# Performance work log

Hardware: AMD Instinct MI355X
Metric: run time of the kernel (lower is better)

Reference implementation:

```python
import jax, jax.numpy as jnp
import numpy as np

N_EMB = 512
EMB_DIM = 64
DECAY = 0.99
EPS = 1e-5


def setup_inputs() -> dict:
    key = jax.random.key(0)
    k1, k2 = jax.random.split(key)
    x = jax.random.normal(k1, (32, EMB_DIM, 64, 64), dtype=jnp.float32)
    weight = jax.random.uniform(k2, (EMB_DIM, N_EMB), dtype=jnp.float32)  # rd_init=True: torch.rand(emb_dim, n_emb)
    cluster_size = jnp.zeros((N_EMB,), dtype=jnp.float32)
    embed_avg = weight  # buffer initialized as embed.clone()
    return {"x": x, "weight": weight, "cluster_size": cluster_size, "embed_avg": embed_avg}


def reference(x, weight, cluster_size, embed_avg):
    B, D, H, W = x.shape
    n_emb = weight.shape[1]
    # (B, D, H, W) -> (N, D) tokens
    flat = jnp.transpose(x, (0, 2, 3, 1)).reshape(-1, D)
    dist = (jnp.sum(flat * flat, axis=1, keepdims=True)
            - 2.0 * (flat @ weight)
            + jnp.sum(weight * weight, axis=0)[None, :])
    argmin = jnp.argmin(dist, axis=1)                      # (N,)
    quant = jnp.take(weight.T, argmin, axis=0)             # gather -> (N, D)
    result = jnp.transpose(quant.reshape(B, H, W, D), (0, 3, 1, 2))  # (B, D, H, W)

    # --- EMA codebook update (training branch) ---
    ones = jnp.ones(argmin.shape, dtype=x.dtype)
    n_idx = jax.ops.segment_sum(ones, argmin, num_segments=n_emb)    # onehot.sum(0)
    n_idx = jnp.where(n_idx == 0, jnp.ones_like(n_idx), n_idx)       # clamp empty clusters to 1
    new_cluster_size = DECAY * cluster_size + (1.0 - DECAY) * n_idx
    embed_sum = jax.ops.segment_sum(flat, argmin, num_segments=n_emb).T  # flatten.T @ onehot -> (D, n_emb)
    new_embed_avg = DECAY * embed_avg + (1.0 - DECAY) * embed_sum
    n = jnp.sum(new_cluster_size)
    cs = (new_cluster_size + EPS) / (n + n_emb * EPS) * n
    new_weight = new_embed_avg / cs[None, :]

    return result, argmin.reshape(B, H, W), new_weight, new_cluster_size, new_embed_avg
```

## Files before the change

kernel.cpp:

```cpp
#include <hip/hip_runtime.h>

#define NEMB 512
#define EMB 64
#define BSTR 262144
#define DECAYF 0.99f
#define OMDF 0.01f
#define EPSF 1e-5f
#define GAP_T 0.012f

typedef __attribute__((ext_vector_type(8))) short bf16x8;
typedef __attribute__((ext_vector_type(4))) float f32x4;

__device__ __forceinline__ unsigned short f2bf(float f) {
    unsigned u = __float_as_uint(f);
    return (unsigned short)((u + 0x7FFFu + ((u >> 16) & 1u)) >> 16);
}
__device__ __forceinline__ float bf2f(unsigned short h) {
    return __uint_as_float(((unsigned)h) << 16);
}

__global__ void prep_kernel(const float* __restrict__ w,
                            unsigned short* __restrict__ wh, unsigned short* __restrict__ wl,
                            float* __restrict__ wsq,
                            float* __restrict__ cnt_ws, float* __restrict__ es_region) {
    int j = threadIdx.x;
    if (blockIdx.x < 8) {
        int d0 = blockIdx.x << 3;
        bf16x8 hb, lb;
#pragma unroll
        for (int i = 0; i < 8; ++i) {
            float v = w[(d0 + i) * NEMB + j];
            unsigned short h = f2bf(v);
            hb[i] = (short)h;
            lb[i] = (short)f2bf(v - bf2f(h));
        }
        *(bf16x8*)(wh + j * EMB + d0) = hb;
        *(bf16x8*)(wl + j * EMB + d0) = lb;
    } else {
        float s = 0.f;
#pragma unroll
        for (int d = 0; d < EMB; ++d) { float v = w[d * NEMB + j]; s = fmaf(v, v, s); }
        wsq[j] = s;
        cnt_ws[j] = 0.f;
#pragma unroll
        for (int k = j; k < 32768; k += 512) es_region[k] = 0.f;
    }
}

#define UPD(S1, J1, S2, J2, s_, j_) do { \
    if (s_ < S1 || (s_ == S1 && j_ < J1)) { S2 = S1; J2 = J1; S1 = s_; J1 = j_; } \
    else if (s_ < S2 || (s_ == S2 && j_ < J2)) { S2 = s_; J2 = j_; } } while (0)

__global__ __launch_bounds__(256, 4) void vq_main(
    const float* __restrict__ x, const float* __restrict__ w,
    const unsigned short* __restrict__ wh, const unsigned short* __restrict__ wl,
    const float* __restrict__ wsq,
    float* __restrict__ out_arg)
{
    __shared__ __align__(16) float xt[EMB * 128];
    __shared__ float xsq_s[128];
    __shared__ float wsq_s[NEMB];
    __shared__ int flg[128];
    __shared__ int nflg;

    const int tid = threadIdx.x;
    const int blk = blockIdx.x;
    const int b  = blk >> 5;
    const int h0 = (blk & 31) << 1;
    const int t0 = b * 4096 + h0 * 64;
    const float* xbase = x + b * BSTR + h0 * 64;

    if (tid == 0) nflg = 0;

#pragma unroll
    for (int it = 0; it < 8; ++it) {
        int idx = tid + (it << 8);
        int d = idx >> 5, q = idx & 31;
        float4 v = *(const float4*)(xbase + d * 4096 + (q << 2));
        *(float4*)(xt + d * 128 + (q << 2)) = v;
    }
    wsq_s[tid] = wsq[tid];
    wsq_s[tid + 256] = wsq[tid + 256];
    __syncthreads();

    if (tid < 128) {
        float s = 0.f;
#pragma unroll
        for (int d = 0; d < EMB; ++d) { float v = xt[d * 128 + tid]; s = fmaf(v, v, s); }
        xsq_s[tid] = s;
    }
    __syncthreads();

    const int lane = tid & 63;
    const int wave = tid >> 6;
    const int l15  = lane & 15;
    const int quad = lane >> 4;
    const int wbase = wave << 5;

    bf16x8 ah[2][2], al[2][2];
#pragma unroll
    for (int mt = 0; mt < 2; ++mt) {
        int m = wbase + (mt << 4) + l15;
#pragma unroll
        for (int ks = 0; ks < 2; ++ks) {
            int k0 = (ks << 5) + (quad << 3);
            bf16x8 hh, ll;
#pragma unroll
            for (int i = 0; i < 8; ++i) {
                float v = xt[(k0 + i) * 128 + m];
                unsigned short h = f2bf(v);
                hh[i] = (short)h;
                ll[i] = (short)f2bf(v - bf2f(h));
            }
            ah[mt][ks] = hh; al[mt][ks] = ll;
        }
    }

    float xq[2][4];
#pragma unroll
    for (int mt = 0; mt < 2; ++mt)
#pragma unroll
        for (int r = 0; r < 4; ++r)
            xq[mt][r] = xsq_s[wbase + (mt << 4) + (quad << 2) + r];

    float v1[2][4], v2[2][4];
    int   j1[2][4];
#pragma unroll
    for (int mt = 0; mt < 2; ++mt)
#pragma unroll
        for (int r = 0; r < 4; ++r) { v1[mt][r] = 3.4e38f; v2[mt][r] = 3.4e38f; j1[mt][r] = 0; }

#pragma unroll 2
    for (int it = 0; it < 32; ++it) {
        const int n = (it << 4) + l15;
        const unsigned short* ph = wh + n * EMB + (quad << 3);
        const unsigned short* pl = wl + n * EMB + (quad << 3);
        bf16x8 b0 = *(const bf16x8*)(ph);
        bf16x8 b1 = *(const bf16x8*)(ph + 32);
        bf16x8 b2 = *(const bf16x8*)(pl);
        bf16x8 b3 = *(const bf16x8*)(pl + 32);
        float wq = wsq_s[n];

        f32x4 acc0 = (f32x4){0.f, 0.f, 0.f, 0.f};
        f32x4 acc1 = (f32x4){0.f, 0.f, 0.f, 0.f};
        acc0 = __builtin_amdgcn_mfma_f32_16x16x32_bf16(ah[0][0], b0, acc0, 0, 0, 0);
        acc1 = __builtin_amdgcn_mfma_f32_16x16x32_bf16(ah[1][0], b0, acc1, 0, 0, 0);
        acc0 = __builtin_amdgcn_mfma_f32_16x16x32_bf16(ah[0][1], b1, acc0, 0, 0, 0);
        acc1 = __builtin_amdgcn_mfma_f32_16x16x32_bf16(ah[1][1], b1, acc1, 0, 0, 0);
        acc0 = __builtin_amdgcn_mfma_f32_16x16x32_bf16(ah[0][0], b2, acc0, 0, 0, 0);
        acc1 = __builtin_amdgcn_mfma_f32_16x16x32_bf16(ah[1][0], b2, acc1, 0, 0, 0);
        acc0 = __builtin_amdgcn_mfma_f32_16x16x32_bf16(ah[0][1], b3, acc0, 0, 0, 0);
        acc1 = __builtin_amdgcn_mfma_f32_16x16x32_bf16(ah[1][1], b3, acc1, 0, 0, 0);
        acc0 = __builtin_amdgcn_mfma_f32_16x16x32_bf16(al[0][0], b0, acc0, 0, 0, 0);
        acc1 = __builtin_amdgcn_mfma_f32_16x16x32_bf16(al[1][0], b0, acc1, 0, 0, 0);
        acc0 = __builtin_amdgcn_mfma_f32_16x16x32_bf16(al[0][1], b1, acc0, 0, 0, 0);
        acc1 = __builtin_amdgcn_mfma_f32_16x16x32_bf16(al[1][1], b1, acc1, 0, 0, 0);

#pragma unroll
        for (int r = 0; r < 4; ++r) {
            float s0 = fmaf(-2.f, acc0[r], xq[0][r] + wq);
            bool p0 = s0 < v1[0][r];
            float mx0 = fmaxf(s0, v1[0][r]);
            v1[0][r] = fminf(s0, v1[0][r]);
            v2[0][r] = fminf(v2[0][r], mx0);
            j1[0][r] = p0 ? n : j1[0][r];

            float s1 = fmaf(-2.f, acc1[r], xq[1][r] + wq);
            bool p1 = s1 < v1[1][r];
            float mx1 = fmaxf(s1, v1[1][r]);
            v1[1][r] = fminf(s1, v1[1][r]);
            v2[1][r] = fminf(v2[1][r], mx1);
            j1[1][r] = p1 ? n : j1[1][r];
        }
    }

#pragma unroll
    for (int mt = 0; mt < 2; ++mt)
#pragma unroll
        for (int r = 0; r < 4; ++r) {
            float a1 = v1[mt][r], a2 = v2[mt][r];
            int   aj = j1[mt][r];
#pragma unroll
            for (int msk = 1; msk < 16; msk <<= 1) {
                float o1 = __shfl_xor(a1, msk, 64);
                int   oj = __shfl_xor(aj, msk, 64);
                float o2 = __shfl_xor(a2, msk, 64);
                bool take = (o1 < a1) || (o1 == a1 && oj < aj);
                float mx = fmaxf(a1, o1);
                a2 = fminf(fminf(a2, o2), mx);
                a1 = fminf(a1, o1);
                aj = take ? oj : aj;
            }
            v1[mt][r] = a1; v2[mt][r] = a2; j1[mt][r] = aj;
        }

    if (l15 == 0) {
#pragma unroll
        for (int mt = 0; mt < 2; ++mt)
#pragma unroll
            for (int r = 0; r < 4; ++r) {
                int mlocal = wbase + (mt << 4) + (quad << 2) + r;
                out_arg[t0 + mlocal] = (float)j1[mt][r];
                if (v2[mt][r] - v1[mt][r] < GAP_T) {
                    int idx = atomicAdd(&nflg, 1);
                    flg[idx] = mlocal;
                }
            }
    }
    __syncthreads();

    const int nf = nflg;
    for (int g = wave; g < nf; g += 4) {
        const int m = flg[g];
        float xd = xt[lane * 128 + m];
        float xqv = xd * xd;
#pragma unroll
        for (int mk = 1; mk < 64; mk <<= 1) xqv += __shfl_xor(xqv, mk, 64);

        float accv[8];
#pragma unroll
        for (int k = 0; k < 8; ++k) accv[k] = 0.f;
#pragma unroll 4
        for (int d = 0; d < EMB; ++d) {
            float4 wa = *(const float4*)(w + d * NEMB + (lane << 2));
            float4 wb = *(const float4*)(w + d * NEMB + 256 + (lane << 2));
            float xv = __shfl(xd, d, 64);
            accv[0] = fmaf(xv, wa.x, accv[0]);
            accv[1] = fmaf(xv, wa.y, accv[1]);
            accv[2] = fmaf(xv, wa.z, accv[2]);
            accv[3] = fmaf(xv, wa.w, accv[3]);
            accv[4] = fmaf(xv, wb.x, accv[4]);
            accv[5] = fmaf(xv, wb.y, accv[5]);
            accv[6] = fmaf(xv, wb.z, accv[6]);
            accv[7] = fmaf(xv, wb.w, accv[7]);
        }

        float S1 = 3.4e38f, S2 = 3.4e38f; int J1 = 0, J2 = 0;
#pragma unroll
        for (int k = 0; k < 8; ++k) {
            int j = (k < 4) ? ((lane << 2) + k) : (256 + (lane << 2) + k - 4);
            float s = (xqv - 2.f * accv[k]) + wsq_s[j];
            UPD(S1, J1, S2, J2, s, j);
        }
#pragma unroll
        for (int mk = 1; mk < 64; mk <<= 1) {
            float os1 = __shfl_xor(S1, mk, 64); int oj1 = __shfl_xor(J1, mk, 64);
            float os2 = __shfl_xor(S2, mk, 64); int oj2 = __shfl_xor(J2, mk, 64);
            UPD(S1, J1, S2, J2, os1, oj1);
            UPD(S1, J1, S2, J2, os2, oj2);
        }

        int jm = J1;
        if (S2 - S1 < 1e-3f) {
            float w1 = w[lane * NEMB + J1];
            float w2 = w[lane * NEMB + J2];
            double e1 = (double)w1 * (double)w1 - 2.0 * (double)xd * (double)w1;
            double e2 = (double)w2 * (double)w2 - 2.0 * (double)xd * (double)w2;
#pragma unroll
            for (int mk = 1; mk < 64; mk <<= 1) {
                e1 += __shfl_xor(e1, mk, 64);
                e2 += __shfl_xor(e2, mk, 64);
            }
            if (e2 < e1 || (e2 == e1 && J2 < J1)) jm = J2;
        }
        if (lane == 0) out_arg[t0 + m] = (float)jm;
    }
}

__global__ __launch_bounds__(256) void finish_kernel(
    const float* __restrict__ x, const float* __restrict__ w, const float* __restrict__ arg,
    float* __restrict__ out_result,
    float* __restrict__ es, float* __restrict__ cnt)
{
    __shared__ float wrow[NEMB];
    __shared__ float acc[NEMB];
    const int tid = threadIdx.x;
    const int grp = blockIdx.x >> 5;
    const int chunk = blockIdx.x & 31;

    acc[tid] = 0.f; acc[tid + 256] = 0.f;
    if (grp < 64) {
        wrow[tid] = w[grp * NEMB + tid];
        wrow[tid + 256] = w[grp * NEMB + tid + 256];
    }
    __syncthreads();

    const int tbase = chunk << 12;
    if (grp < 64) {
        const int d = grp;
#pragma unroll 2
        for (int it = 0; it < 4; ++it) {
            int t = tbase + (it << 10) + (tid << 2);
            int o = (t >> 12) * BSTR + d * 4096 + (t & 4095);
            float4 a4 = *(const float4*)(arg + t);
            float4 x4 = *(const float4*)(x + o);
            int j0 = (int)a4.x, j1 = (int)a4.y, j2 = (int)a4.z, j3 = (int)a4.w;
            atomicAdd(&acc[j0], x4.x);
            atomicAdd(&acc[j1], x4.y);
            atomicAdd(&acc[j2], x4.z);
            atomicAdd(&acc[j3], x4.w);
            float4 r4 = {wrow[j0], wrow[j1], wrow[j2], wrow[j3]};
            *(float4*)(out_result + o) = r4;
        }
    } else {
#pragma unroll 2
        for (int it = 0; it < 4; ++it) {
            int t = tbase + (it << 10) + (tid << 2);
            float4 a4 = *(const float4*)(arg + t);
            atomicAdd(&acc[(int)a4.x], 1.0f);
            atomicAdd(&acc[(int)a4.y], 1.0f);
            atomicAdd(&acc[(int)a4.z], 1.0f);
            atomicAdd(&acc[(int)a4.w], 1.0f);
        }
    }
    __syncthreads();

    float* dst = (grp < 64) ? (es + grp * NEMB) : cnt;
#pragma unroll
    for (int k = 0; k < 2; ++k) {
        int j = tid + (k << 8);
        float v = acc[j];
        if (v != 0.f) atomicAdd(&dst[j], v);
    }
}

__global__ void finalize_kernel(const float* __restrict__ cs_in, const float* __restrict__ avg_in,
                                const float* __restrict__ cnt_ws,
                                float* __restrict__ out_w, float* __restrict__ out_ncs,
                                float* __restrict__ avg_io ) {
    __shared__ float red[NEMB];
    const int j = threadIdx.x;
    const int d = blockIdx.x;
    float c = cnt_ws[j];
    float nidx = (c == 0.f) ? 1.f : c;
    float ncs = DECAYF * cs_in[j] + OMDF * nidx;
    red[j] = ncs;
    __syncthreads();
    for (int s = 256; s > 0; s >>= 1) {
        if (j < s) red[j] += red[j + s];
        __syncthreads();
    }
    float n = red[0];
    float csj = (ncs + EPSF) / (n + (float)NEMB * EPSF) * n;
    int o = d * NEMB + j;
    float esv = avg_io[o];
    float navg = DECAYF * avg_in[o] + OMDF * esv;
    avg_io[o] = navg;
    out_w[o] = navg / csj;
    if (d == 0) out_ncs[j] = ncs;
}

extern "C" void kernel_launch(void* const* d_in, const int* in_sizes, int n_in,
                              void* d_out, int out_size, void* d_ws, size_t ws_size,
                              hipStream_t stream) {
    (void)in_sizes; (void)n_in; (void)out_size; (void)ws_size;
    const float* x   = (const float*)d_in[0];
    const float* w   = (const float*)d_in[1];
    const float* cs  = (const float*)d_in[2];
    const float* avg = (const float*)d_in[3];

    float* out = (float*)d_out;
    float* out_result = out;
    float* out_arg    = out + 8388608;
    float* out_w      = out + 8519680;
    float* out_ncs    = out + 8552448;
    float* out_avg    = out + 8552960;

    char* wsb = (char*)d_ws;
    unsigned short* wh = (unsigned short*)wsb;
    unsigned short* wl = (unsigned short*)(wsb + 65536);
    float* wsq      = (float*)(wsb + 131072);
    float* cnt_ws   = (float*)(wsb + 133120);

    prep_kernel<<<9, 512, 0, stream>>>(w, wh, wl, wsq, cnt_ws, out_avg);
    vq_main<<<1024, 256, 0, stream>>>(x, w, wh, wl, wsq, out_arg);
    finish_kernel<<<2080, 256, 0, stream>>>(x, w, out_arg, out_result, out_avg, cnt_ws);
    finalize_kernel<<<64, 512, 0, stream>>>(cs, avg, cnt_ws, out_w, out_ncs, out_avg);
}
```

Before: 211.8 us.

## Split VQ refinement into a global-queue kernel and privatize histogram bins

vq_main drops LDS staging of the x tile. Each block now handles one 64-token row with 128 threads, loading x directly into bf16 hi/lo fragments, computing ||x||^2 with shuffles, and prefetching the next codebook fragments in registers. Tokens with ambiguous argmin are pushed to a capped global queue and re-checked in fp32 by a new refine_kernel, instead of inside each block. finish_kernel spreads its LDS atomics over 8 padded copies of the histogram to reduce bank and address contention. The trade-offs are an extra launch, a global atomic counter, less coalesced strided x loads, and silently dropped refinements if the queue cap is ever exceeded.

```diff
diff --git a/kernel.cpp b/kernel.cpp
--- a/kernel.cpp
+++ b/kernel.cpp
@@ -7,6 +7,7 @@
 #define OMDF 0.01f
 #define EPSF 1e-5f
 #define GAP_T 0.012f
+#define QCAP 32768
 
 typedef __attribute__((ext_vector_type(8))) short bf16x8;
 typedef __attribute__((ext_vector_type(4))) float f32x4;
@@ -22,7 +23,8 @@
 __global__ void prep_kernel(const float* __restrict__ w,
                             unsigned short* __restrict__ wh, unsigned short* __restrict__ wl,
                             float* __restrict__ wsq,
-                            float* __restrict__ cnt_ws, float* __restrict__ es_region) {
+                            float* __restrict__ cnt_ws, float* __restrict__ es_region,
+                            unsigned* __restrict__ gcnt) {
     int j = threadIdx.x;
     if (blockIdx.x < 8) {
         int d0 = blockIdx.x << 3;
@@ -42,6 +44,7 @@
         for (int d = 0; d < EMB; ++d) { float v = w[d * NEMB + j]; s = fmaf(v, v, s); }
         wsq[j] = s;
         cnt_ws[j] = 0.f;
+        if (j == 0) *gcnt = 0u;
 #pragma unroll
         for (int k = j; k < 32768; k += 512) es_region[k] = 0.f;
     }
@@ -51,45 +54,25 @@
     if (s_ < S1 || (s_ == S1 && j_ < J1)) { S2 = S1; J2 = J1; S1 = s_; J1 = j_; } \
     else if (s_ < S2 || (s_ == S2 && j_ < J2)) { S2 = s_; J2 = j_; } } while (0)
 
-__global__ __launch_bounds__(256, 4) void vq_main(
-    const float* __restrict__ x, const float* __restrict__ w,
+__global__ __launch_bounds__(128, 4) void vq_main(
+    const float* __restrict__ x,
     const unsigned short* __restrict__ wh, const unsigned short* __restrict__ wl,
     const float* __restrict__ wsq,
-    float* __restrict__ out_arg)
+    float* __restrict__ out_arg, unsigned* __restrict__ gcnt, int* __restrict__ queue)
 {
-    __shared__ __align__(16) float xt[EMB * 128];
-    __shared__ float xsq_s[128];
     __shared__ float wsq_s[NEMB];
-    __shared__ int flg[128];
-    __shared__ int nflg;
 
     const int tid = threadIdx.x;
     const int blk = blockIdx.x;
-    const int b  = blk >> 5;
-    const int h0 = (blk & 31) << 1;
-    const int t0 = b * 4096 + h0 * 64;
-    const float* xbase = x + b * BSTR + h0 * 64;
-
-    if (tid == 0) nflg = 0;
-
-#pragma unroll
-    for (int it = 0; it < 8; ++it) {
-        int idx = tid + (it << 8);
-        int d = idx >> 5, q = idx & 31;
-        float4 v = *(const float4*)(xbase + d * 4096 + (q << 2));
-        *(float4*)(xt + d * 128 + (q << 2)) = v;
-    }
-    wsq_s[tid] = wsq[tid];
+    const int b   = blk >> 6;
+    const int h   = blk & 63;
+    const int t0  = b * 4096 + h * 64;
+    const float* xrow = x + b * BSTR + h * 64;
+
+    wsq_s[tid]       = wsq[tid];
+    wsq_s[tid + 128] = wsq[tid + 128];
     wsq_s[tid + 256] = wsq[tid + 256];
-    __syncthreads();
-
-    if (tid < 128) {
-        float s = 0.f;
-#pragma unroll
-        for (int d = 0; d < EMB; ++d) { float v = xt[d * 128 + tid]; s = fmaf(v, v, s); }
-        xsq_s[tid] = s;
-    }
-    __syncthreads();
+    wsq_s[tid + 384] = wsq[tid + 384];
 
     const int lane = tid & 63;
     const int wave = tid >> 6;
@@ -98,30 +81,32 @@
     const int wbase = wave << 5;
 
     bf16x8 ah[2][2], al[2][2];
+    float  xq[2][4];
 #pragma unroll
     for (int mt = 0; mt < 2; ++mt) {
-        int m = wbase + (mt << 4) + l15;
+        const float* xp = xrow + wbase + (mt << 4) + l15;
+        float s = 0.f;
 #pragma unroll
         for (int ks = 0; ks < 2; ++ks) {
-            int k0 = (ks << 5) + (quad << 3);
+            const int d0 = (ks << 5) + (quad << 3);
             bf16x8 hh, ll;
 #pragma unroll
             for (int i = 0; i < 8; ++i) {
-                float v = xt[(k0 + i) * 128 + m];
-                unsigned short h = f2bf(v);
-                hh[i] = (short)h;
-                ll[i] = (short)f2bf(v - bf2f(h));
+                float v = xp[(d0 + i) * 4096];
+                s = fmaf(v, v, s);
+                unsigned short hb = f2bf(v);
+                hh[i] = (short)hb;
+                ll[i] = (short)f2bf(v - bf2f(hb));
             }
             ah[mt][ks] = hh; al[mt][ks] = ll;
         }
-    }
-
-    float xq[2][4];
-#pragma unroll
-    for (int mt = 0; mt < 2; ++mt)
+        s += __shfl_xor(s, 16, 64);
+        s += __shfl_xor(s, 32, 64);
 #pragma unroll
         for (int r = 0; r < 4; ++r)
-            xq[mt][r] = xsq_s[wbase + (mt << 4) + (quad << 2) + r];
+            xq[mt][r] = __shfl(s, (quad << 2) + r, 64);
+    }
+    __syncthreads();
 
     float v1[2][4], v2[2][4];
     int   j1[2][4];
@@ -130,15 +115,24 @@
 #pragma unroll
         for (int r = 0; r < 4; ++r) { v1[mt][r] = 3.4e38f; v2[mt][r] = 3.4e38f; j1[mt][r] = 0; }
 
+    const unsigned short* ph = wh + l15 * EMB + (quad << 3);
+    const unsigned short* pl = wl + l15 * EMB + (quad << 3);
+    bf16x8 nb0 = *(const bf16x8*)(ph);
+    bf16x8 nb1 = *(const bf16x8*)(ph + 32);
+    bf16x8 nb2 = *(const bf16x8*)(pl);
+    bf16x8 nb3 = *(const bf16x8*)(pl + 32);
+
 #pragma unroll 2
     for (int it = 0; it < 32; ++it) {
+        bf16x8 b0 = nb0, b1 = nb1, b2 = nb2, b3 = nb3;
+        if (it != 31) {
+            ph += 1024; pl += 1024;
+            nb0 = *(const bf16x8*)(ph);
+            nb1 = *(const bf16x8*)(ph + 32);
+            nb2 = *(const bf16x8*)(pl);
+            nb3 = *(const bf16x8*)(pl + 32);
+        }
         const int n = (it << 4) + l15;
-        const unsigned short* ph = wh + n * EMB + (quad << 3);
-        const unsigned short* pl = wl + n * EMB + (quad << 3);
-        bf16x8 b0 = *(const bf16x8*)(ph);
-        bf16x8 b1 = *(const bf16x8*)(ph + 32);
-        bf16x8 b2 = *(const bf16x8*)(pl);
-        bf16x8 b3 = *(const bf16x8*)(pl + 32);
         float wq = wsq_s[n];
 
         f32x4 acc0 = (f32x4){0.f, 0.f, 0.f, 0.f};
@@ -199,20 +193,36 @@
         for (int mt = 0; mt < 2; ++mt)
 #pragma unroll
             for (int r = 0; r < 4; ++r) {
-                int mlocal = wbase + (mt << 4) + (quad << 2) + r;
-                out_arg[t0 + mlocal] = (float)j1[mt][r];
+                int gt = t0 + wbase + (mt << 4) + (quad << 2) + r;
+                out_arg[gt] = (float)j1[mt][r];
                 if (v2[mt][r] - v1[mt][r] < GAP_T) {
-                    int idx = atomicAdd(&nflg, 1);
-                    flg[idx] = mlocal;
+                    unsigned idx = atomicAdd(gcnt, 1u);
+                    if (idx < QCAP) queue[idx] = gt;
                 }
             }
     }
-    __syncthreads();
-
-    const int nf = nflg;
-    for (int g = wave; g < nf; g += 4) {
-        const int m = flg[g];
-        float xd = xt[lane * 128 + m];
+}
+
+__global__ __launch_bounds__(256) void refine_kernel(
+    const float* __restrict__ x, const float* __restrict__ w,
+    const float* __restrict__ wsq, const unsigned* __restrict__ gcnt,
+    const int* __restrict__ queue, float* __restrict__ out_arg)
+{
+    __shared__ float wsq_s[NEMB];
+    const int tid = threadIdx.x;
+    wsq_s[tid] = wsq[tid];
+    wsq_s[tid + 256] = wsq[tid + 256];
+    __syncthreads();
+
+    unsigned nfu = *gcnt;
+    const int nf = (int)(nfu < (unsigned)QCAP ? nfu : (unsigned)QCAP);
+    const int lane = tid & 63;
+    const int gw = (blockIdx.x << 2) + (tid >> 6);
+
+    for (int i = gw; i < nf; i += 1024) {
+        const int t = queue[i];
+        const int b = t >> 12, pos = t & 4095;
+        float xd = x[b * BSTR + lane * 4096 + pos];
         float xqv = xd * xd;
 #pragma unroll
         for (int mk = 1; mk < 64; mk <<= 1) xqv += __shfl_xor(xqv, mk, 64);
@@ -263,7 +273,7 @@
             }
             if (e2 < e1 || (e2 == e1 && J2 < J1)) jm = J2;
         }
-        if (lane == 0) out_arg[t0 + m] = (float)jm;
+        if (lane == 0) out_arg[t] = (float)jm;
     }
 }
 
@@ -273,18 +283,21 @@
     float* __restrict__ es, float* __restrict__ cnt)
 {
     __shared__ float wrow[NEMB];
-    __shared__ float acc[NEMB];
+    __shared__ float acc[8][513];
     const int tid = threadIdx.x;
     const int grp = blockIdx.x >> 5;
     const int chunk = blockIdx.x & 31;
 
-    acc[tid] = 0.f; acc[tid + 256] = 0.f;
+    float* af = &acc[0][0];
+#pragma unroll
+    for (int k = tid; k < 8 * 513; k += 256) af[k] = 0.f;
     if (grp < 64) {
         wrow[tid] = w[grp * NEMB + tid];
         wrow[tid + 256] = w[grp * NEMB + tid + 256];
     }
     __syncthreads();
 
+    const int c = tid & 7;
     const int tbase = chunk << 12;
     if (grp < 64) {
         const int d = grp;
@@ -295,10 +308,10 @@
             float4 a4 = *(const float4*)(arg + t);
             float4 x4 = *(const float4*)(x + o);
             int j0 = (int)a4.x, j1 = (int)a4.y, j2 = (int)a4.z, j3 = (int)a4.w;
-            atomicAdd(&acc[j0], x4.x);
-            atomicAdd(&acc[j1], x4.y);
-            atomicAdd(&acc[j2], x4.z);
-            atomicAdd(&acc[j3], x4.w);
+            atomicAdd(&acc[c][j0], x4.x);
+            atomicAdd(&acc[c][j1], x4.y);
+            atomicAdd(&acc[c][j2], x4.z);
+            atomicAdd(&acc[c][j3], x4.w);
             float4 r4 = {wrow[j0], wrow[j1], wrow[j2], wrow[j3]};
             *(float4*)(out_result + o) = r4;
         }
@@ -307,10 +320,10 @@
         for (int it = 0; it < 4; ++it) {
             int t = tbase + (it << 10) + (tid << 2);
             float4 a4 = *(const float4*)(arg + t);
-            atomicAdd(&acc[(int)a4.x], 1.0f);
-            atomicAdd(&acc[(int)a4.y], 1.0f);
-            atomicAdd(&acc[(int)a4.z], 1.0f);
-            atomicAdd(&acc[(int)a4.w], 1.0f);
+            atomicAdd(&acc[c][(int)a4.x], 1.0f);
+            atomicAdd(&acc[c][(int)a4.y], 1.0f);
+            atomicAdd(&acc[c][(int)a4.z], 1.0f);
+            atomicAdd(&acc[c][(int)a4.w], 1.0f);
         }
     }
     __syncthreads();
@@ -319,7 +332,8 @@
 #pragma unroll
     for (int k = 0; k < 2; ++k) {
         int j = tid + (k << 8);
-        float v = acc[j];
+        float v = acc[0][j] + acc[1][j] + acc[2][j] + acc[3][j]
+                + acc[4][j] + acc[5][j] + acc[6][j] + acc[7][j];
         if (v != 0.f) atomicAdd(&dst[j], v);
     }
 }
@@ -371,9 +385,12 @@
     unsigned short* wl = (unsigned short*)(wsb + 65536);
     float* wsq      = (float*)(wsb + 131072);
     float* cnt_ws   = (float*)(wsb + 133120);
-
-    prep_kernel<<<9, 512, 0, stream>>>(w, wh, wl, wsq, cnt_ws, out_avg);
-    vq_main<<<1024, 256, 0, stream>>>(x, w, wh, wl, wsq, out_arg);
+    unsigned* gcnt  = (unsigned*)(wsb + 135168);
+    int* queue      = (int*)(wsb + 135232);
+
+    prep_kernel<<<9, 512, 0, stream>>>(w, wh, wl, wsq, cnt_ws, out_avg, gcnt);
+    vq_main<<<2048, 128, 0, stream>>>(x, wh, wl, wsq, out_arg, gcnt, queue);
+    refine_kernel<<<256, 256, 0, stream>>>(x, w, wsq, gcnt, queue, out_arg);
     finish_kernel<<<2080, 256, 0, stream>>>(x, w, out_arg, out_result, out_avg, cnt_ws);
     finalize_kernel<<<64, 512, 0, stream>>>(cs, avg, cnt_ws, out_w, out_ncs, out_avg);
 }
```

Result: no change. 214.3 us (+1.2%).
